# Kernel optimization log

Measured on AMD Instinct MI355X. Metric: run time of the kernel, lower is better.

## Reference

```python
import jax, jax.numpy as jnp
import numpy as np

V, MAXLEN, D, I, C, L, S = 32000, 4096, 1024, 4096, 1024, 4, 4096


def setup_inputs() -> dict:
    key = jax.random.key(0)
    ks = jax.random.split(key, 20)
    sd = 0.02
    inp = {
        "input_indices": jax.random.randint(ks[0], (S,), 0, V),
        "emb": jax.random.normal(ks[1], (V, D), jnp.float32) * sd,
        "pos": jax.random.normal(ks[2], (MAXLEN, D), jnp.float32) * sd,
        "Wq": jax.random.normal(ks[3], (L, D, I), jnp.float32) * sd,
        "bq": jnp.zeros((L, I), jnp.float32),
        "Wk": jax.random.normal(ks[4], (L, D, I), jnp.float32) * sd,
        "bk": jnp.zeros((L, I), jnp.float32),
        "Wv": jax.random.normal(ks[5], (L, D, I), jnp.float32) * sd,
        "bv": jnp.zeros((L, I), jnp.float32),
        "Wo": jax.random.normal(ks[6], (L, I, D), jnp.float32) * sd,
        "bo": jnp.zeros((L, D), jnp.float32),
        "W1": jax.random.normal(ks[7], (L, D, I), jnp.float32) * sd,
        "b1": jnp.zeros((L, I), jnp.float32),
        "W2": jax.random.normal(ks[8], (L, I, D), jnp.float32) * sd,
        "b2": jnp.zeros((L, D), jnp.float32),
        "Wout": jax.random.normal(ks[9], (D, C), jnp.float32) * sd,
        "bout": jnp.zeros((C,), jnp.float32),
    }
    return inp


def reference(input_indices, emb, pos, Wq, bq, Wk, bk, Wv, bv, Wo, bo, W1, b1, W2, b2, Wout, bout):
    s = input_indices.shape[0]
    x = emb[input_indices] + pos[:s]  # [S, D]
    causal_mask = jnp.triu(jnp.ones((s, s), bool), k=1)  # True above diagonal -> masked
    scale = 1.0 / np.sqrt(Wq.shape[-1]).astype(np.float32)

    def layer(x, p):
        wq, bq_, wk, bk_, wv, bv_, wo, bo_, w1, b1_, w2, b2_ = p
        q = x @ wq + bq_  # [S, I]
        k = x @ wk + bk_
        v = x @ wv + bv_
        scores = (q @ k.T) * scale  # [S, S]
        scores = jnp.where(causal_mask, -jnp.inf, scores)
        attn = jax.nn.softmax(scores, axis=-1)
        r = x + (attn @ v) @ wo + bo_  # residual + attention output projection
        f = jnp.maximum(r @ w1 + b1_, 0.0) @ w2 + b2_  # ReLU FFN
        return r + f, attn

    x, attention_maps = jax.lax.scan(
        layer, x, (Wq, bq, Wk, bk, Wv, bv, Wo, bo, W1, b1, W2, b2)
    )
    logits = x @ Wout + bout  # [S, C]
    log_probs = jax.nn.log_softmax(logits, axis=-1)
    return log_probs, attention_maps  # [S, C], [L, S, S]
```

## Files before the change

kernel.cpp:

```cpp
#include <hip/hip_runtime.h>
#include <stdint.h>
#include <math.h>

#define S_ 4096
#define D_ 1024
#define I_ 4096
#define C_ 1024
#define L_ 4

typedef unsigned short u16;
typedef short bf16x8 __attribute__((ext_vector_type(8)));
typedef float f32x4 __attribute__((ext_vector_type(4)));

__device__ __forceinline__ u16 f2bf(float f) {
  union { float f; uint32_t u; } c; c.f = f;
  return (u16)((c.u + 0x7FFFu + ((c.u >> 16) & 1u)) >> 16);
}
__device__ __forceinline__ float bf2f(u16 b) {
  union { uint32_t u; float f; } c; c.u = (uint32_t)b << 16;
  return c.f;
}
__device__ __forceinline__ u16 f2h(float f) {
  _Float16 h = (_Float16)f;
  return *(u16*)&h;
}
__device__ __forceinline__ float h2f(u16 b) {
  _Float16 h = *(_Float16*)&b;
  return (float)h;
}

__device__ __forceinline__ void gll16(const void* g, void* l) {
  __builtin_amdgcn_global_load_lds(
      (__attribute__((address_space(1))) void*)(g),
      (__attribute__((address_space(3))) void*)(l), 16, 0, 0);
}

#define BAR() asm volatile("s_barrier" ::: "memory")
#define WAITV(n) asm volatile("s_waitcnt vmcnt(" #n ")" ::: "memory")

__device__ __forceinline__ int xcd_swz(int orig, int nwg) {
  int q8 = nwg >> 3, r8 = nwg & 7;
  int xcd = orig & 7, rem = orig >> 3;
  return (xcd < r8 ? xcd * (q8 + 1) : r8 * (q8 + 1) + (xcd - r8) * q8) + rem;
}

__device__ __forceinline__ void gemm256_body(
    u16* sA, u16* sB,
    const u16* __restrict__ A, const u16* __restrict__ Bt,
    const float* __restrict__ bias, const float* __restrict__ resid,
    float* __restrict__ outF, u16* __restrict__ outB, u16* __restrict__ outH,
    u16* __restrict__ outT, int ldT,
    int N, int K, float scale, int relu,
    int row0, int col0, int t0, int t1)
{
  int tid = threadIdx.x, l = tid & 63;
  int w = tid >> 6;
  int wr = w >> 2, wc = w & 3;
  int lrow = l & 15, lq = l >> 4;
  int hb = wc >> 1;
  int rx = lrow & 7;

  const u16* ap[2]; const u16* bp[2]; int dst[2];
#pragma unroll
  for (int u = 0; u < 2; ++u) {
    int c = u * 512 + tid;
    int row = c >> 3;
    int oct = (c & 7) ^ (row & 7);
    ap[u] = A + (size_t)(row0 + row) * K + oct * 8;
    bp[u] = Bt + (size_t)(col0 + row) * K + oct * 8;
    dst[u] = c * 8;
  }

#define STAGE_A(par, hh, t)                                                     \
  { _Pragma("unroll") for (int u = 0; u < 2; ++u)                               \
      gll16(ap[u] + (size_t)(hh) * 128 * K + (t) * 64,                          \
            &sA[((par) * 2 + (hh)) * 8192 + dst[u]]); }
#define STAGE_B(par, hh, t)                                                     \
  { _Pragma("unroll") for (int u = 0; u < 2; ++u)                               \
      gll16(bp[u] + (size_t)(hh) * 128 * K + (t) * 64,                          \
            &sB[((par) * 2 + (hh)) * 8192 + dst[u]]); }
#define LD_A(DST, par, mh)                                                      \
  { _Pragma("unroll") for (int mi = 0; mi < 4; ++mi)                            \
    _Pragma("unroll") for (int kc = 0; kc < 2; ++kc)                            \
      DST[mi][kc] = *(const bf16x8*)&sA[((par) * 2 + wr) * 8192 +               \
          ((mh) * 64 + mi * 16 + lrow) * 64 + (((kc * 4 + lq) ^ rx) * 8)]; }
#define LD_B(DST, par, nh)                                                      \
  { _Pragma("unroll") for (int nj = 0; nj < 2; ++nj)                            \
    _Pragma("unroll") for (int kc = 0; kc < 2; ++kc)                            \
      DST[nj][kc] = *(const bf16x8*)&sB[((par) * 2 + hb) * 8192 +               \
          ((wc & 1) * 64 + (nh) * 32 + nj * 16 + lrow) * 64 +                   \
          (((kc * 4 + lq) ^ rx) * 8)]; }

  f32x4 acc[8][4];
#pragma unroll
  for (int i = 0; i < 8; ++i)
#pragma unroll
    for (int j = 0; j < 4; ++j) {
      acc[i][j][0] = 0.f; acc[i][j][1] = 0.f; acc[i][j][2] = 0.f; acc[i][j][3] = 0.f;
    }

#define MM(AF, MB, NB)                                                          \
  { __builtin_amdgcn_s_setprio(1);                                             \
    _Pragma("unroll") for (int kc = 0; kc < 2; ++kc)                            \
    _Pragma("unroll") for (int mi = 0; mi < 4; ++mi)                            \
    _Pragma("unroll") for (int nj = 0; nj < 2; ++nj)                            \
      acc[(MB) + mi][(NB) + nj] = __builtin_amdgcn_mfma_f32_16x16x32_bf16(      \
          AF[mi][kc], bfv[nj][kc], acc[(MB) + mi][(NB) + nj], 0, 0, 0);         \
    __builtin_amdgcn_s_setprio(0); }

  bf16x8 afA[4][2], afB[4][2], bfv[2][2];

  STAGE_A(0, 0, t0); STAGE_A(0, 1, t0); STAGE_B(0, 0, t0); STAGE_B(0, 1, t0);
  STAGE_A(1, 0, t0 + 1); STAGE_A(1, 1, t0 + 1); STAGE_B(1, 0, t0 + 1);
  WAITV(6);
  BAR();

  for (int t = t0; t < t1; ++t) {
    int p = (t - t0) & 1;
    LD_A(afA, p, 0);
    LD_B(bfv, p, 0);
    LD_A(afB, p, 1);
    if (t + 1 < t1) STAGE_B(p ^ 1, 1, t + 1);
    BAR();
    MM(afA, 0, 0);
    BAR();
    if (t + 2 < t1) STAGE_A(p, 0, t + 2);
    BAR();
    MM(afB, 4, 0);
    BAR();
    LD_B(bfv, p, 1);
    if (t + 2 < t1) STAGE_A(p, 1, t + 2);
    BAR();
    MM(afB, 4, 2);
    BAR();
    if (t + 2 < t1) STAGE_B(p, 0, t + 2);
    BAR();
    MM(afA, 0, 2);
    if (t + 2 < t1) { WAITV(6); } else { WAITV(0); }
    BAR();
  }
#undef STAGE_A
#undef STAGE_B
#undef LD_A
#undef LD_B
#undef MM

  float biasv[4] = {0.f, 0.f, 0.f, 0.f};
  if (bias) {
#pragma unroll
    for (int j = 0; j < 4; ++j) biasv[j] = bias[col0 + wc * 64 + j * 16 + lrow];
  }

  if (outT) {
    u16* tlds = sA;
    int myhalf = wc >> 1;
    int colb = tid >> 5;
    int sub = tid & 31;
#pragma unroll
    for (int half = 0; half < 2; ++half) {
      BAR();
      if (myhalf == half) {
#pragma unroll
        for (int i = 0; i < 8; ++i)
#pragma unroll
          for (int r = 0; r < 4; ++r)
#pragma unroll
            for (int j = 0; j < 4; ++j) {
              int cl = (wc * 64 + j * 16 + lrow) & 127;
              int rowl = wr * 128 + i * 16 + lq * 4 + r;
              tlds[cl * 264 + rowl] = f2bf(acc[i][j][r] + biasv[j]);
            }
      }
      BAR();
#pragma unroll
      for (int it = 0; it < 8; ++it) {
        int cl = it * 16 + colb;
        size_t gb = (size_t)(col0 + half * 128 + cl) * ldT + row0 + sub * 8;
        bf16x8 v = *(const bf16x8*)&tlds[cl * 264 + sub * 8];
        *(bf16x8*)&outT[gb] = v;
      }
    }
    return;
  }

#pragma unroll
  for (int i = 0; i < 8; ++i) {
#pragma unroll
    for (int r = 0; r < 4; ++r) {
      int row = row0 + wr * 128 + i * 16 + lq * 4 + r;
      size_t ro = (size_t)row * N;
#pragma unroll
      for (int j = 0; j < 4; ++j) {
        int col = col0 + wc * 64 + j * 16 + lrow;
        float v = acc[i][j][r] * scale + biasv[j];
        if (resid) v += resid[ro + col];
        if (relu) v = fmaxf(v, 0.f);
        if (outF) outF[ro + col] = v;
        if (outB) outB[ro + col] = f2bf(v);
        if (outH) outH[ro + col] = f2h(v);
      }
    }
  }
}

__global__ __launch_bounds__(512, 2) void gemm256k(
    const u16* __restrict__ A, const u16* __restrict__ Bt,
    const float* __restrict__ bias, const float* __restrict__ resid,
    float* __restrict__ outF, u16* __restrict__ outB,
    int M, int N, int K, float scale, int flags, int k0, int k1)
{
  extern __shared__ char smem[];
  int wg = xcd_swz(blockIdx.x, gridDim.x);
  int nbx = N / 256;
  int br = wg / nbx, bc = wg % nbx;
  gemm256_body((u16*)smem, (u16*)smem + 32768, A, Bt, bias, resid, outF, outB,
               nullptr, nullptr, 0, N, K, scale, flags & 1, br * 256, bc * 256,
               k0 / 64, k1 / 64);
}

struct B3 { const float* b[3]; };
__global__ __launch_bounds__(512, 2) void gemm256_qkv(
    const u16* __restrict__ A, const u16* __restrict__ BtBase,
    B3 b3, u16* __restrict__ outQK, u16* __restrict__ vT, int K)
{
  extern __shared__ char smem[];
  int wg = xcd_swz(blockIdx.x, gridDim.x);
  int z = wg >> 8;
  int tile = wg & 255;
  int br = tile >> 4, bc = tile & 15;
  if (z < 2) {
    gemm256_body((u16*)smem, (u16*)smem + 32768, A,
                 BtBase + (size_t)z * I_ * D_, b3.b[z], nullptr,
                 nullptr, outQK + (size_t)z * S_ * I_, nullptr, nullptr, 0,
                 I_, K, 1.0f, 0, br * 256, bc * 256, 0, K / 64);
  } else {
    gemm256_body((u16*)smem, (u16*)smem + 32768, A,
                 BtBase + (size_t)2 * I_ * D_, b3.b[2], nullptr,
                 nullptr, nullptr, nullptr, vT, S_,
                 I_, K, 1.0f, 0, br * 256, bc * 256, 0, K / 64);
  }
}

__global__ __launch_bounds__(512, 2) void gemm256_tri3(
    const u16* __restrict__ A, const u16* __restrict__ Bt,
    u16* __restrict__ out0, u16* __restrict__ out1, u16* __restrict__ out2,
    int K, float scale)
{
  extern __shared__ char smem[];
  int wg = xcd_swz(blockIdx.x, gridDim.x);
  int ntri = gridDim.x / 3;
  int chunk = wg / ntri;
  int tile = wg - chunk * ntri;
  int br = (int)((sqrtf(8.0f * (float)tile + 1.0f) - 1.0f) * 0.5f);
  while ((br + 1) * (br + 2) / 2 <= tile) ++br;
  while (br * (br + 1) / 2 > tile) --br;
  int bc = tile - br * (br + 1) / 2;
  int t0 = (chunk == 0) ? 0 : (chunk == 1 ? 22 : 43);
  int t1 = (chunk == 0) ? 22 : (chunk == 1 ? 43 : 64);
  u16* o = (chunk == 0) ? out0 : (chunk == 1 ? out1 : out2);
  gemm256_body((u16*)smem, (u16*)smem + 32768, A, Bt, nullptr, nullptr,
               nullptr, nullptr, o, nullptr, 0,
               S_, K, scale, 0, br * 256, bc * 256, t0, t1);
}

__global__ __launch_bounds__(512, 2) void gemm256_pv(
    const u16* __restrict__ A, const u16* __restrict__ Bt,
    u16* __restrict__ outB, u16* __restrict__ pvH)
{
  extern __shared__ char smem[];
  int wg = xcd_swz(blockIdx.x, gridDim.x);
  if (wg < 128) {
    int br = wg >> 4, bc = wg & 15;
    gemm256_body((u16*)smem, (u16*)smem + 32768, A, Bt, nullptr, nullptr,
                 nullptr, outB, nullptr, nullptr, 0, I_, S_, 1.0f, 0,
                 br * 256, bc * 256, 0, (br + 1) * 4);
  } else {
    int c = wg - 128;
    int br = 8 + (c >> 5);
    int bc = (c >> 1) & 15;
    int chunk = c & 1;
    int lim = (br + 1) * 4;
    int half = lim >> 1;
    u16* o = pvH + (size_t)chunk * (S_ / 2) * I_ - (size_t)2048 * I_;
    gemm256_body((u16*)smem, (u16*)smem + 32768, A, Bt, nullptr, nullptr,
                 nullptr, nullptr, o, nullptr, 0, I_, S_, 1.0f, 0,
                 br * 256, bc * 256, chunk ? half : 0, chunk ? lim : half);
  }
}

__global__ __launch_bounds__(256) void combine2pv(
    const u16* __restrict__ pvH, u16* __restrict__ outB)
{
  const int MN = (S_ / 2) * I_;
  int i = (blockIdx.x * 256 + threadIdx.x) * 4;
  ushort4 a = *(const ushort4*)&pvH[i];
  ushort4 b = *(const ushort4*)&pvH[MN + i];
  ushort4 o;
  o.x = f2bf(h2f(a.x) + h2f(b.x));
  o.y = f2bf(h2f(a.y) + h2f(b.y));
  o.z = f2bf(h2f(a.z) + h2f(b.z));
  o.w = f2bf(h2f(a.w) + h2f(b.w));
  *(ushort4*)&outB[(size_t)2048 * I_ + i] = o;
}

__global__ __launch_bounds__(512, 2) void gemm256_ks4(
    const u16* __restrict__ A, const u16* __restrict__ Bt,
    u16* __restrict__ pOut, int M, int N, int K)
{
  extern __shared__ char smem[];
  int wg = xcd_swz(blockIdx.x, gridDim.x);
  int chunk = wg & 3;
  int tile = wg >> 2;
  int nbx = N / 256;
  int br = tile / nbx, bc = tile % nbx;
  u16* o = pOut + (size_t)chunk * M * N;
  int kq = K / 4;
  gemm256_body((u16*)smem, (u16*)smem + 32768, A, Bt, nullptr, nullptr,
               nullptr, nullptr, o, nullptr, 0, N, K, 1.0f, 0,
               br * 256, bc * 256, (chunk * kq) / 64, ((chunk + 1) * kq) / 64);
}

__global__ __launch_bounds__(256) void combine4(
    const u16* __restrict__ p, const float* __restrict__ bias,
    const u16* __restrict__ residB, u16* __restrict__ outB, int MN, int N)
{
  int i = (blockIdx.x * 256 + threadIdx.x) * 4;
  ushort4 a = *(const ushort4*)&p[i];
  ushort4 b = *(const ushort4*)&p[MN + i];
  ushort4 c = *(const ushort4*)&p[2 * MN + i];
  ushort4 d = *(const ushort4*)&p[3 * MN + i];
  ushort4 rb = *(const ushort4*)&residB[i];
  f32x4 v;
  v[0] = h2f(a.x) + h2f(b.x) + h2f(c.x) + h2f(d.x) + bf2f(rb.x);
  v[1] = h2f(a.y) + h2f(b.y) + h2f(c.y) + h2f(d.y) + bf2f(rb.y);
  v[2] = h2f(a.z) + h2f(b.z) + h2f(c.z) + h2f(d.z) + bf2f(rb.z);
  v[3] = h2f(a.w) + h2f(b.w) + h2f(c.w) + h2f(d.w) + bf2f(rb.w);
  int col = i & (N - 1);
  v += *(const f32x4*)&bias[col];
  ushort4 o;
  o.x = f2bf(v[0]); o.y = f2bf(v[1]); o.z = f2bf(v[2]); o.w = f2bf(v[3]);
  *(ushort4*)&outB[i] = o;
}

struct T6 {
  const float* src[6];
  u16* dst[6];
};

__global__ __launch_bounds__(256) void trans6_f2b(T6 a) {
  __shared__ float tile[64][65];
  int z = blockIdx.z;
  bool big = (z == 3 || z == 5);
  int R = big ? I_ : D_;
  int C = big ? D_ : I_;
  int bid = blockIdx.y * gridDim.x + blockIdx.x;
  int nbx = C / 64;
  int bx = bid % nbx, by = bid / nbx;
  const float* src = a.src[z];
  u16* dst = a.dst[z];
  int c0 = bx * 64, r0 = by * 64;
  int tx = threadIdx.x & 63, ty = threadIdx.x >> 6;
#pragma unroll
  for (int i = 0; i < 64; i += 4)
    tile[ty + i][tx] = src[(size_t)(r0 + ty + i) * C + c0 + tx];
  __syncthreads();
#pragma unroll
  for (int i = 0; i < 64; i += 4)
    dst[(size_t)(c0 + ty + i) * R + r0 + tx] = f2bf(tile[tx][ty + i]);
}

__global__ __launch_bounds__(256) void trans_f2b(const float* __restrict__ src,
                                                 u16* __restrict__ dst, int R, int C)
{
  __shared__ float tile[32][33];
  int c0 = blockIdx.x * 32, r0 = blockIdx.y * 32;
  int tx = threadIdx.x & 31, ty = threadIdx.x >> 5;
#pragma unroll
  for (int i = 0; i < 32; i += 8)
    tile[ty + i][tx] = src[(size_t)(r0 + ty + i) * C + c0 + tx];
  __syncthreads();
#pragma unroll
  for (int i = 0; i < 32; i += 8)
    dst[(size_t)(c0 + ty + i) * R + r0 + tx] = f2bf(tile[tx][ty + i]);
}

__global__ __launch_bounds__(256) void embed_k(const int* __restrict__ idx,
                                               const float* __restrict__ emb,
                                               const float* __restrict__ pos,
                                               u16* __restrict__ xb)
{
  int i = (blockIdx.x * 256 + threadIdx.x) * 8;
  int s = i >> 10;
  int d = i & (D_ - 1);
  const float* e = emb + (size_t)idx[s] * D_ + d;
  const float* p = pos + (size_t)s * D_ + d;
  f32x4 v0 = *(const f32x4*)e + *(const f32x4*)p;
  f32x4 v1 = *(const f32x4*)(e + 4) + *(const f32x4*)(p + 4);
  ushort4 b0, b1;
  b0.x = f2bf(v0[0]); b0.y = f2bf(v0[1]); b0.z = f2bf(v0[2]); b0.w = f2bf(v0[3]);
  b1.x = f2bf(v1[0]); b1.y = f2bf(v1[1]); b1.z = f2bf(v1[2]); b1.w = f2bf(v1[3]);
  *(ushort4*)&xb[i] = b0;
  *(ushort4*)&xb[i + 4] = b1;
}

__global__ __launch_bounds__(256) void softmax_causal(float* __restrict__ att,
                                                      const u16* __restrict__ p0,
                                                      const u16* __restrict__ p1,
                                                      const u16* __restrict__ p2,
                                                      u16* __restrict__ attB)
{
  int s = blockIdx.x;
  __shared__ float row[S_];
  __shared__ float red[8];
  int tid = threadIdx.x, l = tid & 63, w = tid >> 6;
  int nv = s + 1;
  size_t base = (size_t)s * S_;
  float m = -3.0e38f;
  for (int c = tid; c < nv; c += 256) {
    float v = h2f(p0[base + c]) + h2f(p1[base + c]) + h2f(p2[base + c]);
    row[c] = v; m = fmaxf(m, v);
  }
#pragma unroll
  for (int off = 32; off; off >>= 1) m = fmaxf(m, __shfl_xor(m, off, 64));
  if (l == 0) red[w] = m;
  __syncthreads();
  m = fmaxf(fmaxf(red[0], red[1]), fmaxf(red[2], red[3]));
  float sum = 0.f;
  for (int c = tid; c < nv; c += 256) { float e = __expf(row[c] - m); row[c] = e; sum += e; }
#pragma unroll
  for (int off = 32; off; off >>= 1) sum += __shfl_xor(sum, off, 64);
  if (l == 0) red[4 + w] = sum;
  __syncthreads();
  sum = red[4] + red[5] + red[6] + red[7];
  float inv = 1.0f / sum;
  int nb = ((s >> 8) + 1) * 256;
  for (int c = tid; c < S_; c += 256) {
    float p = (c < nv) ? row[c] * inv : 0.0f;
    att[base + c] = p;
    if (c < nb) attB[base + c] = f2bf(p);
  }
}

__global__ __launch_bounds__(256) void logsoftmax_k(const u16* __restrict__ p,
                                                    const float* __restrict__ bias,
                                                    float* __restrict__ out)
{
  const int MN = S_ * C_;
  int s = blockIdx.x;
  int tid = threadIdx.x, l = tid & 63, w = tid >> 6;
  __shared__ float red[8];
  size_t base = (size_t)s * C_;
  float v[4];
  float m = -3.0e38f;
#pragma unroll
  for (int k = 0; k < 4; ++k) {
    int col = tid + k * 256;
    size_t i = base + col;
    v[k] = h2f(p[i]) + h2f(p[MN + i]) + h2f(p[2 * MN + i]) + h2f(p[3 * MN + i])
           + bias[col];
    m = fmaxf(m, v[k]);
  }
#pragma unroll
  for (int off = 32; off; off >>= 1) m = fmaxf(m, __shfl_xor(m, off, 64));
  if (l == 0) red[w] = m;
  __syncthreads();
  m = fmaxf(fmaxf(red[0], red[1]), fmaxf(red[2], red[3]));
  float sum = 0.f;
#pragma unroll
  for (int k = 0; k < 4; ++k) sum += __expf(v[k] - m);
#pragma unroll
  for (int off = 32; off; off >>= 1) sum += __shfl_xor(sum, off, 64);
  if (l == 0) red[4 + w] = sum;
  __syncthreads();
  sum = red[4] + red[5] + red[6] + red[7];
  float lz = logf(sum);
#pragma unroll
  for (int k = 0; k < 4; ++k) out[base + tid + k * 256] = v[k] - m - lz;
}

extern "C" void kernel_launch(void* const* d_in, const int* in_sizes, int n_in,
                              void* d_out, int out_size, void* d_ws, size_t ws_size,
                              hipStream_t stream) {
  (void)in_sizes; (void)n_in; (void)out_size; (void)ws_size;
  const int*   idx  = (const int*)d_in[0];
  const float* emb  = (const float*)d_in[1];
  const float* pos  = (const float*)d_in[2];
  const float* Wq   = (const float*)d_in[3];
  const float* bq   = (const float*)d_in[4];
  const float* Wk   = (const float*)d_in[5];
  const float* bk   = (const float*)d_in[6];
  const float* Wv   = (const float*)d_in[7];
  const float* bv   = (const float*)d_in[8];
  const float* Wo   = (const float*)d_in[9];
  const float* bo   = (const float*)d_in[10];
  const float* W1   = (const float*)d_in[11];
  const float* b1   = (const float*)d_in[12];
  const float* W2   = (const float*)d_in[13];
  const float* b2   = (const float*)d_in[14];
  const float* Wout = (const float*)d_in[15];
  const float* bout = (const float*)d_in[16];
  float* out = (float*)d_out;

  char* ws = (char*)d_ws;
  const size_t MB = 1024ull * 1024ull;
  u16*  xbf    = (u16*)(ws + 16 * MB);
  u16*  bufQ   = (u16*)(ws + 24 * MB);
  u16*  bufK   = (u16*)(ws + 56 * MB);
  u16*  bufVT  = (u16*)(ws + 120 * MB);
  u16*  attnB  = (u16*)(ws + 152 * MB);
  u16* WqT   = (u16*)(ws + 200 * MB);
  u16* WkT   = (u16*)(ws + 208 * MB);
  u16* WvT   = (u16*)(ws + 216 * MB);
  u16* WoT   = (u16*)(ws + 224 * MB);
  u16* W1T   = (u16*)(ws + 232 * MB);
  u16* W2T   = (u16*)(ws + 240 * MB);
  u16* WoutT = (u16*)(ws + 248 * MB);
  u16* attP0 = (u16*)(ws + 256 * MB);
  u16* attP1 = (u16*)(ws + 288 * MB);
  u16* attP2 = (u16*)(ws + 320 * MB);
  u16* shP   = (u16*)(ws + 352 * MB);

  const float iscale = 1.0f / 64.0f;
  const int LDSB = 131072;
  hipFuncSetAttribute((const void*)gemm256k,
                      hipFuncAttributeMaxDynamicSharedMemorySize, LDSB);
  hipFuncSetAttribute((const void*)gemm256_qkv,
                      hipFuncAttributeMaxDynamicSharedMemorySize, LDSB);
  hipFuncSetAttribute((const void*)gemm256_tri3,
                      hipFuncAttributeMaxDynamicSharedMemorySize, LDSB);
  hipFuncSetAttribute((const void*)gemm256_pv,
                      hipFuncAttributeMaxDynamicSharedMemorySize, LDSB);
  hipFuncSetAttribute((const void*)gemm256_ks4,
                      hipFuncAttributeMaxDynamicSharedMemorySize, LDSB);
  const int G_SQ = (S_ / 256) * (I_ / 256);

  embed_k<<<(S_ * D_) / (256 * 8), 256, 0, stream>>>(idx, emb, pos, xbf);

  for (int layer = 0; layer < L_; ++layer) {
    T6 t6;
    t6.src[0] = Wq + (size_t)layer * D_ * I_; t6.dst[0] = WqT;
    t6.src[1] = Wk + (size_t)layer * D_ * I_; t6.dst[1] = WkT;
    t6.src[2] = Wv + (size_t)layer * D_ * I_; t6.dst[2] = WvT;
    t6.src[3] = Wo + (size_t)layer * I_ * D_; t6.dst[3] = WoT;
    t6.src[4] = W1 + (size_t)layer * D_ * I_; t6.dst[4] = W1T;
    t6.src[5] = W2 + (size_t)layer * I_ * D_; t6.dst[5] = W2T;
    trans6_f2b<<<dim3(64, 16, 6), 256, 0, stream>>>(t6);

    B3 b3;
    b3.b[0] = bq + (size_t)layer * I_;
    b3.b[1] = bk + (size_t)layer * I_;
    b3.b[2] = bv + (size_t)layer * I_;
    gemm256_qkv<<<3 * G_SQ, 512, LDSB, stream>>>(xbf, WqT, b3, bufQ, bufVT, D_);

    float* attL = out + (size_t)S_ * C_ + (size_t)layer * S_ * S_;
    gemm256_tri3<<<3 * 136, 512, LDSB, stream>>>(bufQ, bufK, attP0, attP1, attP2,
                                                 I_, iscale);

    softmax_causal<<<S_, 256, 0, stream>>>(attL, attP0, attP1, attP2, attnB);

    gemm256_pv<<<384, 512, LDSB, stream>>>(attnB, bufVT, bufQ, shP);
    combine2pv<<<(S_ / 2) * (I_ / 1024), 256, 0, stream>>>(shP, bufQ);

    gemm256_ks4<<<(S_ / 256) * (D_ / 256) * 4, 512, LDSB, stream>>>(
        bufQ, WoT, shP, S_, D_, I_);
    combine4<<<(S_ * D_) / 1024, 256, 0, stream>>>(
        shP, bo + (size_t)layer * D_, xbf, xbf, S_ * D_, D_);

    gemm256k<<<G_SQ, 512, LDSB, stream>>>(
        xbf, W1T, b1 + (size_t)layer * I_, nullptr, nullptr, bufK,
        S_, I_, D_, 1.0f, 1, 0, D_);

    gemm256_ks4<<<(S_ / 256) * (D_ / 256) * 4, 512, LDSB, stream>>>(
        bufK, W2T, shP, S_, D_, I_);
    combine4<<<(S_ * D_) / 1024, 256, 0, stream>>>(
        shP, b2 + (size_t)layer * D_, xbf, xbf, S_ * D_, D_);
  }

  trans_f2b<<<dim3(C_ / 32, D_ / 32), 256, 0, stream>>>(Wout, WoutT, D_, C_);
  gemm256_ks4<<<(S_ / 256) * (C_ / 256) * 4, 512, LDSB, stream>>>(
      xbf, WoutT, shP, S_, C_, D_);
  logsoftmax_k<<<S_, 256, 0, stream>>>(shP, bout, out);
}
```

Measured before the change: 2.100 ms.

## Stage GEMM epilogue through LDS for vectorized stores; split QK^T into two chunks

The scattered per-element GEMM epilogue stores (outF/outB/outH with resid) are replaced by an LDS-staged path. Each half of the 256x256 tile is written to shared memory and then stored as 16-byte rows, giving coalesced global writes. Separately, the causal QK^T split-K is reduced from three chunks to two, so softmax reads one fewer partial buffer and there is less fp16 partial traffic. The trade-off is extra barriers and LDS reuse in the epilogue, and fewer, longer workgroups for the score GEMM, which may lower occupancy or load balance.

```diff
diff --git a/kernel.cpp b/kernel.cpp
--- a/kernel.cpp
+++ b/kernel.cpp
@@ -47,8 +47,8 @@
 __device__ __forceinline__ void gemm256_body(
     u16* sA, u16* sB,
     const u16* __restrict__ A, const u16* __restrict__ Bt,
-    const float* __restrict__ bias, const float* __restrict__ resid,
-    float* __restrict__ outF, u16* __restrict__ outB, u16* __restrict__ outH,
+    const float* __restrict__ bias,
+    u16* __restrict__ outU, int isBF,
     u16* __restrict__ outT, int ldT,
     int N, int K, float scale, int relu,
     int row0, int col0, int t0, int t1)
@@ -183,38 +183,48 @@
     return;
   }
 
-#pragma unroll
-  for (int i = 0; i < 8; ++i) {
-#pragma unroll
-    for (int r = 0; r < 4; ++r) {
-      int row = row0 + wr * 128 + i * 16 + lq * 4 + r;
-      size_t ro = (size_t)row * N;
-#pragma unroll
-      for (int j = 0; j < 4; ++j) {
-        int col = col0 + wc * 64 + j * 16 + lrow;
-        float v = acc[i][j][r] * scale + biasv[j];
-        if (resid) v += resid[ro + col];
-        if (relu) v = fmaxf(v, 0.f);
-        if (outF) outF[ro + col] = v;
-        if (outB) outB[ro + col] = f2bf(v);
-        if (outH) outH[ro + col] = f2h(v);
-      }
+  u16* tlds = sA;
+  int rl0 = tid >> 5;
+  int ch = tid & 31;
+#pragma unroll
+  for (int half = 0; half < 2; ++half) {
+    BAR();
+    if (wr == half) {
+#pragma unroll
+      for (int i = 0; i < 8; ++i)
+#pragma unroll
+        for (int r = 0; r < 4; ++r)
+#pragma unroll
+          for (int j = 0; j < 4; ++j) {
+            int rowl = i * 16 + lq * 4 + r;
+            int cl = wc * 64 + j * 16 + lrow;
+            float v = acc[i][j][r] * scale + biasv[j];
+            if (relu) v = fmaxf(v, 0.f);
+            tlds[rowl * 264 + cl] = isBF ? f2bf(v) : f2h(v);
+          }
+    }
+    BAR();
+#pragma unroll
+    for (int it = 0; it < 8; ++it) {
+      int rowl = it * 16 + rl0;
+      size_t gb = (size_t)(row0 + half * 128 + rowl) * N + col0 + ch * 8;
+      bf16x8 v = *(const bf16x8*)&tlds[rowl * 264 + ch * 8];
+      *(bf16x8*)&outU[gb] = v;
     }
   }
 }
 
 __global__ __launch_bounds__(512, 2) void gemm256k(
     const u16* __restrict__ A, const u16* __restrict__ Bt,
-    const float* __restrict__ bias, const float* __restrict__ resid,
-    float* __restrict__ outF, u16* __restrict__ outB,
+    const float* __restrict__ bias, u16* __restrict__ outB,
     int M, int N, int K, float scale, int flags, int k0, int k1)
 {
   extern __shared__ char smem[];
   int wg = xcd_swz(blockIdx.x, gridDim.x);
   int nbx = N / 256;
   int br = wg / nbx, bc = wg % nbx;
-  gemm256_body((u16*)smem, (u16*)smem + 32768, A, Bt, bias, resid, outF, outB,
-               nullptr, nullptr, 0, N, K, scale, flags & 1, br * 256, bc * 256,
+  gemm256_body((u16*)smem, (u16*)smem + 32768, A, Bt, bias, outB, 1,
+               nullptr, 0, N, K, scale, flags & 1, br * 256, bc * 256,
                k0 / 64, k1 / 64);
 }
 
@@ -230,36 +240,36 @@
   int br = tile >> 4, bc = tile & 15;
   if (z < 2) {
     gemm256_body((u16*)smem, (u16*)smem + 32768, A,
-                 BtBase + (size_t)z * I_ * D_, b3.b[z], nullptr,
-                 nullptr, outQK + (size_t)z * S_ * I_, nullptr, nullptr, 0,
+                 BtBase + (size_t)z * I_ * D_, b3.b[z],
+                 outQK + (size_t)z * S_ * I_, 1, nullptr, 0,
                  I_, K, 1.0f, 0, br * 256, bc * 256, 0, K / 64);
   } else {
     gemm256_body((u16*)smem, (u16*)smem + 32768, A,
-                 BtBase + (size_t)2 * I_ * D_, b3.b[2], nullptr,
-                 nullptr, nullptr, nullptr, vT, S_,
+                 BtBase + (size_t)2 * I_ * D_, b3.b[2],
+                 nullptr, 1, vT, S_,
                  I_, K, 1.0f, 0, br * 256, bc * 256, 0, K / 64);
   }
 }
 
-__global__ __launch_bounds__(512, 2) void gemm256_tri3(
+__global__ __launch_bounds__(512, 2) void gemm256_tri2(
     const u16* __restrict__ A, const u16* __restrict__ Bt,
-    u16* __restrict__ out0, u16* __restrict__ out1, u16* __restrict__ out2,
+    u16* __restrict__ out0, u16* __restrict__ out1,
     int K, float scale)
 {
   extern __shared__ char smem[];
   int wg = xcd_swz(blockIdx.x, gridDim.x);
-  int ntri = gridDim.x / 3;
-  int chunk = wg / ntri;
+  int ntri = gridDim.x >> 1;
+  int chunk = (wg >= ntri) ? 1 : 0;
   int tile = wg - chunk * ntri;
   int br = (int)((sqrtf(8.0f * (float)tile + 1.0f) - 1.0f) * 0.5f);
   while ((br + 1) * (br + 2) / 2 <= tile) ++br;
   while (br * (br + 1) / 2 > tile) --br;
   int bc = tile - br * (br + 1) / 2;
-  int t0 = (chunk == 0) ? 0 : (chunk == 1 ? 22 : 43);
-  int t1 = (chunk == 0) ? 22 : (chunk == 1 ? 43 : 64);
-  u16* o = (chunk == 0) ? out0 : (chunk == 1 ? out1 : out2);
-  gemm256_body((u16*)smem, (u16*)smem + 32768, A, Bt, nullptr, nullptr,
-               nullptr, nullptr, o, nullptr, 0,
+  int t0 = chunk ? 32 : 0;
+  int t1 = chunk ? 64 : 32;
+  u16* o = chunk ? out1 : out0;
+  gemm256_body((u16*)smem, (u16*)smem + 32768, A, Bt, nullptr,
+               o, 0, nullptr, 0,
                S_, K, scale, 0, br * 256, bc * 256, t0, t1);
 }
 
@@ -271,8 +281,8 @@
   int wg = xcd_swz(blockIdx.x, gridDim.x);
   if (wg < 128) {
     int br = wg >> 4, bc = wg & 15;
-    gemm256_body((u16*)smem, (u16*)smem + 32768, A, Bt, nullptr, nullptr,
-                 nullptr, outB, nullptr, nullptr, 0, I_, S_, 1.0f, 0,
+    gemm256_body((u16*)smem, (u16*)smem + 32768, A, Bt, nullptr,
+                 outB, 1, nullptr, 0, I_, S_, 1.0f, 0,
                  br * 256, bc * 256, 0, (br + 1) * 4);
   } else {
     int c = wg - 128;
@@ -282,8 +292,8 @@
     int lim = (br + 1) * 4;
     int half = lim >> 1;
     u16* o = pvH + (size_t)chunk * (S_ / 2) * I_ - (size_t)2048 * I_;
-    gemm256_body((u16*)smem, (u16*)smem + 32768, A, Bt, nullptr, nullptr,
-                 nullptr, nullptr, o, nullptr, 0, I_, S_, 1.0f, 0,
+    gemm256_body((u16*)smem, (u16*)smem + 32768, A, Bt, nullptr,
+                 o, 0, nullptr, 0, I_, S_, 1.0f, 0,
                  br * 256, bc * 256, chunk ? half : 0, chunk ? lim : half);
   }
 }
@@ -315,8 +325,8 @@
   int br = tile / nbx, bc = tile % nbx;
   u16* o = pOut + (size_t)chunk * M * N;
   int kq = K / 4;
-  gemm256_body((u16*)smem, (u16*)smem + 32768, A, Bt, nullptr, nullptr,
-               nullptr, nullptr, o, nullptr, 0, N, K, 1.0f, 0,
+  gemm256_body((u16*)smem, (u16*)smem + 32768, A, Bt, nullptr,
+               o, 0, nullptr, 0, N, K, 1.0f, 0,
                br * 256, bc * 256, (chunk * kq) / 64, ((chunk + 1) * kq) / 64);
 }
 
@@ -406,7 +416,6 @@
 __global__ __launch_bounds__(256) void softmax_causal(float* __restrict__ att,
                                                       const u16* __restrict__ p0,
                                                       const u16* __restrict__ p1,
-                                                      const u16* __restrict__ p2,
                                                       u16* __restrict__ attB)
 {
   int s = blockIdx.x;
@@ -417,7 +426,7 @@
   size_t base = (size_t)s * S_;
   float m = -3.0e38f;
   for (int c = tid; c < nv; c += 256) {
-    float v = h2f(p0[base + c]) + h2f(p1[base + c]) + h2f(p2[base + c]);
+    float v = h2f(p0[base + c]) + h2f(p1[base + c]);
     row[c] = v; m = fmaxf(m, v);
   }
 #pragma unroll
@@ -517,7 +526,6 @@
   u16* WoutT = (u16*)(ws + 248 * MB);
   u16* attP0 = (u16*)(ws + 256 * MB);
   u16* attP1 = (u16*)(ws + 288 * MB);
-  u16* attP2 = (u16*)(ws + 320 * MB);
   u16* shP   = (u16*)(ws + 352 * MB);
 
   const float iscale = 1.0f / 64.0f;
@@ -526,7 +534,7 @@
                       hipFuncAttributeMaxDynamicSharedMemorySize, LDSB);
   hipFuncSetAttribute((const void*)gemm256_qkv,
                       hipFuncAttributeMaxDynamicSharedMemorySize, LDSB);
-  hipFuncSetAttribute((const void*)gemm256_tri3,
+  hipFuncSetAttribute((const void*)gemm256_tri2,
                       hipFuncAttributeMaxDynamicSharedMemorySize, LDSB);
   hipFuncSetAttribute((const void*)gemm256_pv,
                       hipFuncAttributeMaxDynamicSharedMemorySize, LDSB);
@@ -553,10 +561,10 @@
     gemm256_qkv<<<3 * G_SQ, 512, LDSB, stream>>>(xbf, WqT, b3, bufQ, bufVT, D_);
 
     float* attL = out + (size_t)S_ * C_ + (size_t)layer * S_ * S_;
-    gemm256_tri3<<<3 * 136, 512, LDSB, stream>>>(bufQ, bufK, attP0, attP1, attP2,
+    gemm256_tri2<<<2 * 136, 512, LDSB, stream>>>(bufQ, bufK, attP0, attP1,
                                                  I_, iscale);
 
-    softmax_causal<<<S_, 256, 0, stream>>>(attL, attP0, attP1, attP2, attnB);
+    softmax_causal<<<S_, 256, 0, stream>>>(attL, attP0, attP1, attnB);
 
     gemm256_pv<<<384, 512, LDSB, stream>>>(attnB, bufVT, bufQ, shP);
     combine2pv<<<(S_ / 2) * (I_ / 1024), 256, 0, stream>>>(shP, bufQ);
@@ -567,7 +575,7 @@
         shP, bo + (size_t)layer * D_, xbf, xbf, S_ * D_, D_);
 
     gemm256k<<<G_SQ, 512, LDSB, stream>>>(
-        xbf, W1T, b1 + (size_t)layer * I_, nullptr, nullptr, bufK,
+        xbf, W1T, b1 + (size_t)layer * I_, bufK,
         S_, I_, D_, 1.0f, 1, 0, D_);
 
     gemm256_ks4<<<(S_ / 256) * (D_ / 256) * 4, 512, LDSB, stream>>>(
```

Measured after the change: 2.192 ms. 1.04x slower.
